# Kernel optimization log

Measured on AMD Instinct MI355X. Metric: run time of the kernel, lower is better.

## Reference

```python
import jax, jax.numpy as jnp
import numpy as np

DIM = 768
HEADS = 12
HEAD_DIM = DIM // HEADS
GRID = 32
MLP_HIDDEN = DIM * 4
EPS = 1e-5


def layernorm(x, g, b):
    m = jnp.mean(x, axis=-1, keepdims=True)
    v = jnp.mean((x - m) ** 2, axis=-1, keepdims=True)
    return (x - m) * jax.lax.rsqrt(v + EPS) * g + b


def geometry_bias(wg_w, wg_b):
    # Box-relational embedding on a GRIDxGRID grid; batch-invariant so computed once.
    g = GRID
    idx = jnp.arange(g, dtype=jnp.float32)
    px = jnp.repeat(idx, g) / g          # row index, normalized
    py = jnp.tile(idx, g) / g            # col index, normalized
    cx = px + 0.5 / g
    cy = py + 0.5 / g
    wbox = 1.0 + 1.0 / g                 # x_max - x_min + 1 (constant)
    dx = jnp.log(jnp.clip(jnp.abs((cx[:, None] - cx[None, :]) / wbox), 1e-3, None))
    dy = jnp.log(jnp.clip(jnp.abs((cy[:, None] - cy[None, :]) / wbox), 1e-3, None))
    dz = jnp.zeros_like(dx)              # log(w/w) = log(h/h) = 0
    pos = jnp.stack([dx, dy, dz, dz], axis=-1)                      # [N,N,4]
    dim_mat = 1.0 / (1000.0 ** (jnp.arange(8, dtype=jnp.float32) / 8.0))
    mul = (100.0 * pos)[..., None] * dim_mat                        # [N,N,4,8]
    mul = mul.reshape(g * g, g * g, 32)
    emb = jnp.concatenate([jnp.sin(mul), jnp.cos(mul)], axis=-1)    # [N,N,64]
    w = jax.nn.relu(jnp.einsum('ijd,hd->hij', emb, wg_w) + wg_b[:, None, None])
    rgw = jnp.log(jnp.clip(w, 1e-6, None))                          # [H,N,N]
    return jnp.pad(rgw, ((0, 0), (1, 0), (1, 0)))                   # zero row/col for cls


def mha(x, qkv_w, proj_w, proj_b, bias=None):
    Bt, N, C = x.shape
    qkv = (x @ qkv_w.T).reshape(Bt, N, 3, HEADS, HEAD_DIM).transpose(2, 0, 3, 1, 4)
    q, k, v = qkv[0], qkv[1], qkv[2]
    attn = jnp.einsum('bhid,bhjd->bhij', q, k) * (HEAD_DIM ** -0.5)
    if bias is not None:
        attn = attn + bias
    attn = jax.nn.softmax(attn, axis=-1)
    out = jnp.einsum('bhij,bhjd->bhid', attn, v).transpose(0, 2, 1, 3).reshape(Bt, N, C)
    return out @ proj_w.T + proj_b


def mlp(x, fc1_w, fc1_b, fc2_w, fc2_b):
    h = jax.nn.gelu(x @ fc1_w.T + fc1_b, approximate=False)
    return h @ fc2_w.T + fc2_b


def setup_inputs() -> dict:
    key = jax.random.key(0)
    ks = jax.random.split(key, 16)
    s = 0.02
    d = {
        'x': jax.random.normal(ks[0], (2, 4097, DIM), dtype=jnp.float32),
        'norm1_g': jnp.ones((DIM,), jnp.float32), 'norm1_b': jnp.zeros((DIM,), jnp.float32),
        'qkv_w': s * jax.random.normal(ks[1], (3 * DIM, DIM), dtype=jnp.float32),
        'proj_w': s * jax.random.normal(ks[2], (DIM, DIM), dtype=jnp.float32),
        'proj_b': jnp.zeros((DIM,), jnp.float32),
        'wg_w': s * jax.random.normal(ks[3], (HEADS, 64), dtype=jnp.float32),
        'wg_b': s * jax.random.normal(ks[4], (HEADS,), dtype=jnp.float32),
        'tnorm1_g': jnp.ones((DIM,), jnp.float32), 'tnorm1_b': jnp.zeros((DIM,), jnp.float32),
        'tqkv_w': s * jax.random.normal(ks[5], (3 * DIM, DIM), dtype=jnp.float32),
        'tproj_w': s * jax.random.normal(ks[6], (DIM, DIM), dtype=jnp.float32),
        'tproj_b': jnp.zeros((DIM,), jnp.float32),
        'tfc_w': s * jax.random.normal(ks[7], (DIM, DIM), dtype=jnp.float32),
        'tfc_b': jnp.zeros((DIM,), jnp.float32),
        'norm2_g': jnp.ones((DIM,), jnp.float32), 'norm2_b': jnp.zeros((DIM,), jnp.float32),
        'fc1_w': s * jax.random.normal(ks[8], (MLP_HIDDEN, DIM), dtype=jnp.float32),
        'fc1_b': jnp.zeros((MLP_HIDDEN,), jnp.float32),
        'fc2_w': s * jax.random.normal(ks[9], (DIM, MLP_HIDDEN), dtype=jnp.float32),
        'fc2_b': jnp.zeros((DIM,), jnp.float32),
        'B': 2, 'T': 4, 'W': 32,
    }
    return d


def reference(x, norm1_g, norm1_b, qkv_w, proj_w, proj_b, wg_w, wg_b,
              tnorm1_g, tnorm1_b, tqkv_w, tproj_w, tproj_b, tfc_w, tfc_b,
              norm2_g, norm2_b, fc1_w, fc1_b, fc2_w, fc2_b, B, T, W):
    m = x.shape[2]
    H = ((x.shape[1] - 1) // T) // W
    # temporal attention: b (h w t) m -> (b h w) t m
    xt = x[:, 1:, :]
    xt_t = xt.reshape(B, H, W, T, m).reshape(B * H * W, T, m)
    res_t = mha(layernorm(xt_t, tnorm1_g, tnorm1_b), tqkv_w, tproj_w, tproj_b)
    res_t = res_t.reshape(B, H, W, T, m).reshape(B, H * W * T, m)
    res_t = res_t @ tfc_w.T + tfc_b
    xt = x[:, 1:, :] + res_t
    # spatial attention with geometric bias: b (h w t) m -> (b t) (h w) m
    init_cls = x[:, 0:1, :]
    cls = jnp.broadcast_to(init_cls, (B, T, m)).reshape(B * T, 1, m)
    xs = xt.reshape(B, H, W, T, m).transpose(0, 3, 1, 2, 4).reshape(B * T, H * W, m)
    xs = jnp.concatenate([cls, xs], axis=1)
    bias = geometry_bias(wg_w, wg_b)[None]  # [1,heads,1+HW,1+HW]
    res_s = mha(layernorm(xs, norm1_g, norm1_b), qkv_w, proj_w, proj_b, bias=bias)
    cls_out = res_s[:, 0, :].reshape(B, T, m).mean(axis=1, keepdims=True)
    res_s = res_s[:, 1:, :].reshape(B, T, H, W, m).transpose(0, 2, 3, 1, 4).reshape(B, H * W * T, m)
    xout = jnp.concatenate([init_cls, xt], axis=1) + jnp.concatenate([cls_out, res_s], axis=1)
    xout = xout + mlp(layernorm(xout, norm2_g, norm2_b), fc1_w, fc1_b, fc2_w, fc2_b)
    return xout
```

## Files before the change

kernel.cpp:

```cpp
#include <hip/hip_runtime.h>
#include <stdint.h>

#define DIM   768
#define HEADS 12
#define NSP   1025
#define VT_LD 1152
#define PS_LD 136

typedef __attribute__((ext_vector_type(8))) short short8;
typedef __attribute__((ext_vector_type(4))) float f32x4;
typedef unsigned short u16;
typedef unsigned int   u32;

__device__ __forceinline__ u16 f2bf(float v) {
  u32 u = __builtin_bit_cast(u32, v);
  u += 0x7fffu + ((u >> 16) & 1u);
  return (u16)(u >> 16);
}
__device__ __forceinline__ float bf2f(u16 h) {
  u32 u = ((u32)h) << 16;
  return __builtin_bit_cast(float, u);
}

__device__ __forceinline__ void load_lds16(const u16* g, u16* lbase, int lane) {
#if __has_builtin(__builtin_amdgcn_global_load_lds)
  __builtin_amdgcn_global_load_lds((const __attribute__((address_space(1))) void*)g,
                                   (__attribute__((address_space(3))) void*)lbase, 16, 0, 0);
#else
  *(short8*)(lbase + lane * 8) = *(const short8*)g;
#endif
}

__global__ __launch_bounds__(256) void zero_k(float* __restrict__ o, long n) {
  long i = (long)blockIdx.x * 256 + threadIdx.x;
  if (i < n) o[i] = 0.0f;
}

__global__ __launch_bounds__(256) void cvt_k(const float* __restrict__ src,
                                             u16* __restrict__ dst, long n) {
  long i = (long)blockIdx.x * 256 + threadIdx.x;
  if (i < n) dst[i] = f2bf(src[i]);
}

__device__ __forceinline__ void ln_row(const float* __restrict__ src,
                                       u16* __restrict__ dst,
                                       const float* __restrict__ g,
                                       const float* __restrict__ b) {
  int tid = threadIdx.x;
  float v[3];
  float s = 0.f, ss = 0.f;
#pragma unroll
  for (int i = 0; i < 3; i++) {
    v[i] = src[tid + i * 256];
    s += v[i];
    ss += v[i] * v[i];
  }
  __shared__ float red[8];
#pragma unroll
  for (int m = 32; m; m >>= 1) {
    s  += __shfl_xor(s, m);
    ss += __shfl_xor(ss, m);
  }
  int wid = tid >> 6;
  if ((tid & 63) == 0) { red[wid] = s; red[4 + wid] = ss; }
  __syncthreads();
  s  = red[0] + red[1] + red[2] + red[3];
  ss = red[4] + red[5] + red[6] + red[7];
  float mean = s * (1.0f / 768.0f);
  float var  = ss * (1.0f / 768.0f) - mean * mean;
  float rs = rsqrtf(var + 1e-5f);
#pragma unroll
  for (int i = 0; i < 3; i++) {
    int c = tid + i * 256;
    dst[c] = f2bf((v[i] - mean) * rs * g[c] + b[c]);
  }
}

__global__ __launch_bounds__(256) void ln_xt_k(const float* __restrict__ x,
                                               const float* __restrict__ g,
                                               const float* __restrict__ b,
                                               u16* __restrict__ outb) {
  int q = blockIdx.x, bb = blockIdx.y;
  const float* src = x + ((long)bb * 4097 + 1 + q) * DIM;
  u16* dst = outb + ((long)bb * 4096 + q) * DIM;
  ln_row(src, dst, g, b);
}

__global__ __launch_bounds__(256) void ln_xs_k(const float* __restrict__ x,
                                               const float* __restrict__ xt,
                                               const float* __restrict__ g,
                                               const float* __restrict__ b,
                                               u16* __restrict__ outb) {
  int n = blockIdx.x, bt = blockIdx.y;
  int bb = bt >> 2, t = bt & 3;
  const float* src;
  if (n == 0) src = x + (long)bb * 4097 * DIM;
  else        src = xt + ((long)bb * 4096 + (long)(n - 1) * 4 + t) * DIM;
  u16* dst = outb + ((long)bt * NSP + n) * DIM;
  ln_row(src, dst, g, b);
}

__global__ __launch_bounds__(256) void ln2_k(const float* __restrict__ xo,
                                             const float* __restrict__ g,
                                             const float* __restrict__ b,
                                             u16* __restrict__ outb) {
  int n = blockIdx.x, bb = blockIdx.y;
  const float* src = xo + ((long)bb * 4097 + n) * DIM;
  u16* dst = outb + ((long)bb * 4097 + n) * DIM;
  ln_row(src, dst, g, b);
}

struct GemmParams {
  const u16* A; long lda, sA1;
  const u16* B; long ldb;
  void* C;      long ldc, sC1;
  const float* bias;
  const float* resid; long ldr, sR1;
  float scale;
  int M, N, K;
};

template <bool OUTBF16, bool BIASV, bool RESID, bool GELU_>
__global__ __launch_bounds__(256) void gemm_k(GemmParams p) {
  __shared__ u16 As[4096];
  __shared__ u16 Bs[4096];
  int tid = threadIdx.x;
  int z1 = blockIdx.z;
  const u16* A = p.A + (long)z1 * p.sA1;
  const u16* B = p.B;
  int m0 = blockIdx.y * 128, n0 = blockIdx.x * 128;
  int wave = tid >> 6, lane = tid & 63;
  int quad = lane >> 4, lrow = lane & 15;
  int wm = (wave & 1) * 64, wn = (wave >> 1) * 64;

  int rA0 = m0 + (tid >> 2);        if (rA0 > p.M - 1) rA0 = p.M - 1;
  int rA1 = m0 + 64 + (tid >> 2);   if (rA1 > p.M - 1) rA1 = p.M - 1;
  int rB0 = n0 + (tid >> 2);        if (rB0 > p.N - 1) rB0 = p.N - 1;
  int rB1 = n0 + 64 + (tid >> 2);   if (rB1 > p.N - 1) rB1 = p.N - 1;
  int c8 = (tid & 3) << 3;
  const u16* pa0 = A + (long)rA0 * p.lda + c8;
  const u16* pa1 = A + (long)rA1 * p.lda + c8;
  const u16* pb0 = B + (long)rB0 * p.ldb + c8;
  const u16* pb1 = B + (long)rB1 * p.ldb + c8;
  u16* lA0 = As + wave * 512;  u16* lA1 = As + 2048 + wave * 512;
  u16* lB0 = Bs + wave * 512;  u16* lB1 = Bs + 2048 + wave * 512;

  f32x4 acc[4][4];
#pragma unroll
  for (int i = 0; i < 4; i++)
#pragma unroll
    for (int j = 0; j < 4; j++) acc[i][j] = (f32x4){0.f, 0.f, 0.f, 0.f};

  for (int k0 = 0; k0 < p.K; k0 += 32) {
    load_lds16(pa0 + k0, lA0, lane);
    load_lds16(pa1 + k0, lA1, lane);
    load_lds16(pb0 + k0, lB0, lane);
    load_lds16(pb1 + k0, lB1, lane);
    __syncthreads();
    short8 af[4], bfr[4];
#pragma unroll
    for (int i = 0; i < 4; i++) af[i]  = *(const short8*)&As[(wm + i * 16 + lrow) * 32 + quad * 8];
#pragma unroll
    for (int j = 0; j < 4; j++) bfr[j] = *(const short8*)&Bs[(wn + j * 16 + lrow) * 32 + quad * 8];
#pragma unroll
    for (int i = 0; i < 4; i++)
#pragma unroll
      for (int j = 0; j < 4; j++)
        acc[i][j] = __builtin_amdgcn_mfma_f32_16x16x32_bf16(af[i], bfr[j], acc[i][j], 0, 0, 0);
    __syncthreads();
  }

  float* Cf = (float*)p.C;
  u16*   Ch = (u16*)p.C;
  long cbase = (long)z1 * p.sC1;
#pragma unroll
  for (int i = 0; i < 4; i++) {
    int rbase = m0 + wm + i * 16 + quad * 4;
#pragma unroll
    for (int j = 0; j < 4; j++) {
      int c = n0 + wn + j * 16 + lrow;
      if (c >= p.N) continue;
#pragma unroll
      for (int rr = 0; rr < 4; rr++) {
        int r = rbase + rr;
        if (r >= p.M) continue;
        float v = acc[i][j][rr] * p.scale;
        if (BIASV) v += p.bias[c];
        if (GELU_) v = 0.5f * v * (1.0f + erff(v * 0.70710678118654752f));
        if (RESID) v += p.resid[(long)z1 * p.sR1 + (long)r * p.ldr + c];
        long o = cbase + (long)r * p.ldc + c;
        if (OUTBF16) Ch[o] = f2bf(v);
        else         Cf[o] = v;
      }
    }
  }
}

__global__ __launch_bounds__(64) void attn_t_k(const u16* __restrict__ qkv,
                                               u16* __restrict__ outb) {
  int h = blockIdx.x;
  int g = blockIdx.y;
  int d = threadIdx.x;
  long base = (long)g * 4 * 2304 + h * 64 + d;
  float q[4], k[4], vv[4];
#pragma unroll
  for (int t = 0; t < 4; t++) {
    q[t]  = bf2f(qkv[base + (long)t * 2304]);
    k[t]  = bf2f(qkv[base + (long)t * 2304 + 768]);
    vv[t] = bf2f(qkv[base + (long)t * 2304 + 1536]);
  }
  float sc[4][4];
#pragma unroll
  for (int i = 0; i < 4; i++)
#pragma unroll
    for (int j = 0; j < 4; j++) {
      float pv = q[i] * k[j];
#pragma unroll
      for (int m = 32; m; m >>= 1) pv += __shfl_xor(pv, m);
      sc[i][j] = pv * 0.125f;
    }
#pragma unroll
  for (int i = 0; i < 4; i++) {
    float mx = fmaxf(fmaxf(sc[i][0], sc[i][1]), fmaxf(sc[i][2], sc[i][3]));
    float e0 = __expf(sc[i][0] - mx), e1 = __expf(sc[i][1] - mx);
    float e2 = __expf(sc[i][2] - mx), e3 = __expf(sc[i][3] - mx);
    float inv = 1.0f / (e0 + e1 + e2 + e3);
    float ov = (e0 * vv[0] + e1 * vv[1] + e2 * vv[2] + e3 * vv[3]) * inv;
    outb[((long)g * 4 + i) * DIM + h * 64 + d] = f2bf(ov);
  }
}

__global__ void geo_pre_k(const float* __restrict__ wg_w,
                          const float* __restrict__ wg_b,
                          float* __restrict__ sxsyc) {
  int t = threadIdx.x;
  if (t >= 384) return;
  int h = t >> 5, dd = t & 31;
  float dx = logf(fmaxf((float)dd * (1.0f / 33.0f), 0.001f));
  float sx = 0.f, sy = 0.f;
#pragma unroll
  for (int k2 = 0; k2 < 8; k2++) {
    float dm = powf(1000.0f, -(float)k2 / 8.0f);
    float a = 100.0f * dx * dm;
    float sn = sinf(a), cs = cosf(a);
    sx += sn * wg_w[h * 64 + k2]     + cs * wg_w[h * 64 + 32 + k2];
    sy += sn * wg_w[h * 64 + 8 + k2] + cs * wg_w[h * 64 + 40 + k2];
  }
  sxsyc[t] = sx;
  sxsyc[384 + t] = sy;
  if (dd == 0) {
    float c = wg_b[h];
#pragma unroll
    for (int k2 = 48; k2 < 64; k2++) c += wg_w[h * 64 + k2];
    sxsyc[768 + h] = c;
  }
}

__global__ __launch_bounds__(256) void geo_bias_k(const float* __restrict__ sxsyc,
                                                  float* __restrict__ Bh_g) {
  int h = blockIdx.x / 4;
  int idx = (blockIdx.x % 4) * 256 + threadIdx.x;
  int dr = idx >> 5, dc = idx & 31;
  float v = sxsyc[h * 32 + dr] + sxsyc[384 + h * 32 + dc] + sxsyc[768 + h];
  Bh_g[h * 1024 + idx] = logf(fmaxf(fmaxf(v, 0.0f), 1e-6f));
}

__global__ __launch_bounds__(256) void vtrans_k(const u16* __restrict__ qkv_s,
                                                u16* __restrict__ Vt) {
  __shared__ u16 tile[64][33];
  int bh = blockIdx.y;
  int bt = bh / 12, h = bh % 12;
  int j0 = blockIdx.x * 32;
  int tid = threadIdx.x;
#pragma unroll
  for (int it = 0; it < 8; it++) {
    int jj = it * 4 + (tid >> 6);
    int d = tid & 63;
    int j = j0 + jj;
    u16 v = 0;
    if (j < NSP) v = qkv_s[((long)bt * NSP + j) * 2304 + 1536 + h * 64 + d];
    tile[d][jj] = v;
  }
  __syncthreads();
#pragma unroll
  for (int it = 0; it < 8; it++) {
    int d = it * 8 + (tid >> 5);
    int j = tid & 31;
    Vt[((long)bh * 64 + d) * VT_LD + j0 + j] = tile[d][j];
  }
}

__global__ __launch_bounds__(256, 4) void attn_s_k(const u16* __restrict__ qkv,
                                                   const u16* __restrict__ Vt,
                                                   const float* __restrict__ Bh_g,
                                                   u16* __restrict__ attn_o) {
  __shared__ u16 KsF[8192];
  __shared__ u16 UN[8704];
  __shared__ float BhS[1024];
  const int qt = blockIdx.x, bh = blockIdx.y;
  const int bt = bh / 12, h = bh % 12;
  const int tid = threadIdx.x;
  const int wave = tid >> 6, lane = tid & 63;
  const int quad = lane >> 4, lr = lane & 15;
  const int m0 = qt * 64;
  const long qb = (long)bt * NSP * 2304 + h * 64;

#pragma unroll
  for (int i = 0; i < 4; i++) BhS[tid + i * 256] = Bh_g[h * 1024 + tid + i * 256];

  {
    int rowq = tid >> 2, colq = (tid & 3) << 3;
    int tokq = m0 + rowq; if (tokq > 1024) tokq = 1024;
    const u16* gq = qkv + qb + (long)tokq * 2304 + colq;
    load_lds16(gq,      UN + wave * 512, lane);
    load_lds16(gq + 32, UN + 2048 + wave * 512, lane);
  }
  __syncthreads();
  short8 qf[2];
#pragma unroll
  for (int ks = 0; ks < 2; ks++)
    qf[ks] = *(const short8*)&UN[ks * 2048 + (wave * 16 + lr) * 32 + quad * 8];

  f32x4 Oa[4];
  float mr[4], lsum[4];
#pragma unroll
  for (int n = 0; n < 4; n++) Oa[n] = (f32x4){0.f, 0.f, 0.f, 0.f};
#pragma unroll
  for (int r = 0; r < 4; r++) { mr[r] = -1e30f; lsum[r] = 0.f; }

  int rid[4], ri_[4], ci_[4];
  float rok[4];
#pragma unroll
  for (int r = 0; r < 4; r++) {
    int i0 = m0 + wave * 16 + quad * 4 + r;
    rid[r] = i0;
    int ii = i0 < NSP ? i0 : (NSP - 1);
    int im1 = ii > 0 ? ii - 1 : 0;
    ri_[r] = im1 >> 5;
    ci_[r] = im1 & 31;
    rok[r] = (i0 > 0) ? 1.0f : 0.0f;
  }

  int rowk = tid >> 2, colk = (tid & 3) << 3;

  for (int kt = 0; kt < 9; kt++) {
    __syncthreads();
    {
      int t0 = kt * 128 + rowk;      if (t0 > 1024) t0 = 1024;
      int t1 = kt * 128 + 64 + rowk; if (t1 > 1024) t1 = 1024;
      const u16* g0 = qkv + qb + 768 + (long)t0 * 2304 + colk;
      const u16* g1 = qkv + qb + 768 + (long)t1 * 2304 + colk;
      load_lds16(g0,      KsF + wave * 512, lane);
      load_lds16(g1,      KsF + 2048 + wave * 512, lane);
      load_lds16(g0 + 32, KsF + 4096 + wave * 512, lane);
      load_lds16(g1 + 32, KsF + 6144 + wave * 512, lane);
    }
    __syncthreads();
    f32x4 sa[8];
#pragma unroll
    for (int j = 0; j < 8; j++) sa[j] = (f32x4){0.f, 0.f, 0.f, 0.f};
#pragma unroll
    for (int ks = 0; ks < 2; ks++) {
#pragma unroll
      for (int j = 0; j < 8; j++) {
        short8 kf = *(const short8*)&KsF[ks * 4096 + (j * 16 + lr) * 32 + quad * 8];
        sa[j] = __builtin_amdgcn_mfma_f32_16x16x32_bf16(qf[ks], kf, sa[j], 0, 0, 0);
      }
    }
#pragma unroll
    for (int j = 0; j < 8; j++) {
      int j0 = kt * 128 + j * 16 + lr;
      bool jv = j0 < NSP;
      int jm1 = j0 > 0 ? j0 - 1 : 0;
      if (jm1 > 1023) jm1 = 1023;
      int rj = jm1 >> 5, cj = jm1 & 31;
      float jnz = (j0 > 0) ? 1.0f : 0.0f;
#pragma unroll
      for (int r = 0; r < 4; r++) {
        int ad = ri_[r] - rj; ad = ad < 0 ? -ad : ad;
        int cd = ci_[r] - cj; cd = cd < 0 ? -cd : cd;
        float sv = sa[j][r] * 0.125f + BhS[ad * 32 + cd] * jnz * rok[r];
        sa[j][r] = jv ? sv : -1e30f;
      }
    }
    float alpha[4];
#pragma unroll
    for (int r = 0; r < 4; r++) {
      float tm = sa[0][r];
#pragma unroll
      for (int j = 1; j < 8; j++) tm = fmaxf(tm, sa[j][r]);
      tm = fmaxf(tm, __shfl_xor(tm, 1));
      tm = fmaxf(tm, __shfl_xor(tm, 2));
      tm = fmaxf(tm, __shfl_xor(tm, 4));
      tm = fmaxf(tm, __shfl_xor(tm, 8));
      float mn = fmaxf(mr[r], tm);
      float a = __expf(mr[r] - mn);
      alpha[r] = a;
      float ls = 0.f;
      int prow = (wave * 16 + quad * 4 + r) * PS_LD;
#pragma unroll
      for (int j = 0; j < 8; j++) {
        float pp = __expf(sa[j][r] - mn);
        ls += pp;
        UN[prow + j * 16 + lr] = f2bf(pp);
      }
      lsum[r] = lsum[r] * a + ls;
      mr[r] = mn;
    }
#pragma unroll
    for (int n = 0; n < 4; n++)
#pragma unroll
      for (int r = 0; r < 4; r++) Oa[n][r] *= alpha[r];
#pragma unroll
    for (int ks = 0; ks < 4; ks++) {
      short8 pf = *(const short8*)&UN[(wave * 16 + lr) * PS_LD + ks * 32 + quad * 8];
#pragma unroll
      for (int n = 0; n < 4; n++) {
        short8 vf = *(const short8*)(Vt + ((long)bh * 64 + n * 16 + lr) * VT_LD + kt * 128 + ks * 32 + quad * 8);
        Oa[n] = __builtin_amdgcn_mfma_f32_16x16x32_bf16(pf, vf, Oa[n], 0, 0, 0);
      }
    }
  }
#pragma unroll
  for (int r = 0; r < 4; r++) {
    float l = lsum[r];
    l += __shfl_xor(l, 1);
    l += __shfl_xor(l, 2);
    l += __shfl_xor(l, 4);
    l += __shfl_xor(l, 8);
    lsum[r] = 1.0f / l;
  }
#pragma unroll
  for (int r = 0; r < 4; r++) {
    int i0 = rid[r];
    if (i0 < NSP) {
      long ob = ((long)bt * NSP + i0) * 768 + h * 64;
#pragma unroll
      for (int n = 0; n < 4; n++)
        attn_o[ob + n * 16 + lr] = f2bf(Oa[n][r] * lsum[r]);
    }
  }
}

__global__ __launch_bounds__(256) void assemble_k(const float* __restrict__ x,
                                                  const float* __restrict__ xt,
                                                  const float* __restrict__ res_s,
                                                  float* __restrict__ outp) {
  int n = blockIdx.x, bb = blockIdx.y;
  int tid = threadIdx.x;
  long ob = ((long)bb * 4097 + n) * DIM;
  if (n == 0) {
#pragma unroll
    for (int i = 0; i < 3; i++) {
      int c = tid + i * 256;
      float acc = x[ob + c];
#pragma unroll
      for (int t = 0; t < 4; t++)
        acc += 0.25f * res_s[((long)(bb * 4 + t) * NSP) * DIM + c];
      outp[ob + c] = acc;
    }
  } else {
    int q = n - 1, hw = q >> 2, t = q & 3;
    long rs = ((long)(bb * 4 + t) * NSP + 1 + hw) * DIM;
    long xb = ((long)bb * 4096 + q) * DIM;
#pragma unroll
    for (int i = 0; i < 3; i++) {
      int c = tid + i * 256;
      outp[ob + c] = xt[xb + c] + res_s[rs + c];
    }
  }
}

extern "C" void kernel_launch(void* const* d_in, const int* in_sizes, int n_in,
                              void* d_out, int out_size, void* d_ws, size_t ws_size,
                              hipStream_t stream) {
  const float* x        = (const float*)d_in[0];
  const float* norm1_g  = (const float*)d_in[1];
  const float* norm1_b  = (const float*)d_in[2];
  const float* qkv_w    = (const float*)d_in[3];
  const float* proj_w   = (const float*)d_in[4];
  const float* proj_b   = (const float*)d_in[5];
  const float* wg_w     = (const float*)d_in[6];
  const float* wg_b     = (const float*)d_in[7];
  const float* tnorm1_g = (const float*)d_in[8];
  const float* tnorm1_b = (const float*)d_in[9];
  const float* tqkv_w   = (const float*)d_in[10];
  const float* tproj_w  = (const float*)d_in[11];
  const float* tproj_b  = (const float*)d_in[12];
  const float* tfc_w    = (const float*)d_in[13];
  const float* tfc_b    = (const float*)d_in[14];
  const float* norm2_g  = (const float*)d_in[15];
  const float* norm2_b  = (const float*)d_in[16];
  const float* fc1_w    = (const float*)d_in[17];
  const float* fc1_b    = (const float*)d_in[18];
  const float* fc2_w    = (const float*)d_in[19];
  const float* fc2_b    = (const float*)d_in[20];
  float* out = (float*)d_out;
  (void)in_sizes; (void)n_in; (void)out_size;

  char* base = (char*)d_ws;
  size_t off = 0;
  auto take = [&](size_t bytes) -> char* {
    char* p = base + off;
    off += (bytes + 255) & ~(size_t)255;
    return p;
  };

  u16* wb_tqkv = (u16*)take(2304LL * 768 * 2);
  u16* wb_tprj = (u16*)take(768LL * 768 * 2);
  u16* wb_tfc  = (u16*)take(768LL * 768 * 2);
  u16* wb_qkv  = (u16*)take(2304LL * 768 * 2);
  u16* wb_proj = (u16*)take(768LL * 768 * 2);
  u16* wb_fc1  = (u16*)take(3072LL * 768 * 2);
  u16* wb_fc2  = (u16*)take(3072LL * 768 * 2);
  float* xt_f  = (float*)take(8192LL * 768 * 4);
  float* sxsyc = (float*)take(4096);
  float* Bh_g  = (float*)take(12LL * 1024 * 4);
  char* pool   = take(64536576);
  size_t REQ = off;

  u16* qkv_t  = (u16*)(pool);
  u16* ln_xt  = (u16*)(pool + 37748736);
  u16* attn_t = ln_xt;
  u16* h1     = (u16*)(pool + 50331648);
  u16* qkv_s  = (u16*)(pool);
  u16* ln_xs  = (u16*)(pool + 37785600);
  u16* attn_sp = ln_xs;
  u16* Vt     = (u16*)(pool + 50380800);
  float* res_s = (float*)(pool);
  u16* ln2b   = (u16*)(pool);
  u16* geluh  = (u16*)(pool + 12585984);

  if (ws_size < REQ) {
    long n = 2LL * 4097 * 768;
    zero_k<<<dim3((n + 255) / 256), 256, 0, stream>>>(out, n);
    return;
  }

  {
    struct { const float* s; u16* d; long n; } cv[7] = {
      {tqkv_w, wb_tqkv, 2304LL * 768}, {tproj_w, wb_tprj, 768LL * 768},
      {tfc_w, wb_tfc, 768LL * 768},    {qkv_w, wb_qkv, 2304LL * 768},
      {proj_w, wb_proj, 768LL * 768},  {fc1_w, wb_fc1, 3072LL * 768},
      {fc2_w, wb_fc2, 3072LL * 768}};
    for (int i = 0; i < 7; i++)
      cvt_k<<<dim3((cv[i].n + 255) / 256), 256, 0, stream>>>(cv[i].s, cv[i].d, cv[i].n);
  }
  geo_pre_k<<<1, 384, 0, stream>>>(wg_w, wg_b, sxsyc);
  geo_bias_k<<<48, 256, 0, stream>>>(sxsyc, Bh_g);

  ln_xt_k<<<dim3(4096, 2), 256, 0, stream>>>(x, tnorm1_g, tnorm1_b, ln_xt);
  {
    GemmParams p{};
    p.A = ln_xt; p.lda = 768; p.B = wb_tqkv; p.ldb = 768;
    p.C = qkv_t; p.ldc = 2304; p.scale = 1.0f;
    p.M = 8192; p.N = 2304; p.K = 768;
    gemm_k<true, false, false, false><<<dim3(18, 64, 1), 256, 0, stream>>>(p);
  }
  attn_t_k<<<dim3(12, 2048), 64, 0, stream>>>(qkv_t, attn_t);
  {
    GemmParams p{};
    p.A = attn_t; p.lda = 768; p.B = wb_tprj; p.ldb = 768;
    p.C = h1; p.ldc = 768; p.bias = tproj_b; p.scale = 1.0f;
    p.M = 8192; p.N = 768; p.K = 768;
    gemm_k<true, true, false, false><<<dim3(6, 64, 1), 256, 0, stream>>>(p);
  }
  {
    GemmParams p{};
    p.A = h1; p.lda = 768; p.sA1 = 4096LL * 768;
    p.B = wb_tfc; p.ldb = 768;
    p.C = xt_f; p.ldc = 768; p.sC1 = 4096LL * 768;
    p.bias = tfc_b;
    p.resid = x + 768; p.ldr = 768; p.sR1 = 4097LL * 768;
    p.scale = 1.0f;
    p.M = 4096; p.N = 768; p.K = 768;
    gemm_k<false, true, true, false><<<dim3(6, 32, 2), 256, 0, stream>>>(p);
  }

  ln_xs_k<<<dim3(NSP, 8), 256, 0, stream>>>(x, xt_f, norm1_g, norm1_b, ln_xs);
  {
    GemmParams p{};
    p.A = ln_xs; p.lda = 768; p.B = wb_qkv; p.ldb = 768;
    p.C = qkv_s; p.ldc = 2304; p.scale = 1.0f;
    p.M = 8200; p.N = 2304; p.K = 768;
    gemm_k<true, false, false, false><<<dim3(18, 65, 1), 256, 0, stream>>>(p);
  }
  vtrans_k<<<dim3(36, 96), 256, 0, stream>>>(qkv_s, Vt);
  attn_s_k<<<dim3(17, 96), 256, 0, stream>>>(qkv_s, Vt, Bh_g, attn_sp);
  {
    GemmParams p{};
    p.A = attn_sp; p.lda = 768; p.B = wb_proj; p.ldb = 768;
    p.C = res_s; p.ldc = 768; p.bias = proj_b; p.scale = 1.0f;
    p.M = 8200; p.N = 768; p.K = 768;
    gemm_k<false, true, false, false><<<dim3(6, 65, 1), 256, 0, stream>>>(p);
  }
  assemble_k<<<dim3(4097, 2), 256, 0, stream>>>(x, xt_f, res_s, out);

  ln2_k<<<dim3(4097, 2), 256, 0, stream>>>(out, norm2_g, norm2_b, ln2b);
  {
    GemmParams p{};
    p.A = ln2b; p.lda = 768; p.B = wb_fc1; p.ldb = 768;
    p.C = geluh; p.ldc = 3072; p.bias = fc1_b; p.scale = 1.0f;
    p.M = 8194; p.N = 3072; p.K = 768;
    gemm_k<true, true, false, true><<<dim3(24, 65, 1), 256, 0, stream>>>(p);
  }
  {
    GemmParams p{};
    p.A = geluh; p.lda = 3072; p.B = wb_fc2; p.ldb = 3072;
    p.C = out; p.ldc = 768; p.bias = fc2_b;
    p.resid = out; p.ldr = 768; p.scale = 1.0f;
    p.M = 8194; p.N = 768; p.K = 3072;
    gemm_k<false, true, true, false><<<dim3(6, 65, 1), 256, 0, stream>>>(p);
  }
}
```

Before: 818.0 us.

## Add 64-wide GEMM tiles, double-buffer spatial attention K, fuse assemble with LayerNorm

Adds an NT64 GEMM variant with 128x64 output tiles, used for the N=768 projections so they launch more blocks and fill more CUs. The spatial attention kernel now processes 64-key tiles with double-buffered K loads in LDS, prefetches V fragments into registers, and uses a flat grid that interleaves heads across blocks. The residual assemble step is fused with the second LayerNorm, which removes one full read of the output. Risks include a lower MFMA-to-load ratio in the narrow GEMM tiles and an extra barrier on each attention tile iteration.

```diff
diff --git a/kernel.cpp b/kernel.cpp
--- a/kernel.cpp
+++ b/kernel.cpp
@@ -5,7 +5,7 @@
 #define HEADS 12
 #define NSP   1025
 #define VT_LD 1152
-#define PS_LD 136
+#define PS_LD 72
 
 typedef __attribute__((ext_vector_type(8))) short short8;
 typedef __attribute__((ext_vector_type(4))) float f32x4;
@@ -100,16 +100,6 @@
   ln_row(src, dst, g, b);
 }
 
-__global__ __launch_bounds__(256) void ln2_k(const float* __restrict__ xo,
-                                             const float* __restrict__ g,
-                                             const float* __restrict__ b,
-                                             u16* __restrict__ outb) {
-  int n = blockIdx.x, bb = blockIdx.y;
-  const float* src = xo + ((long)bb * 4097 + n) * DIM;
-  u16* dst = outb + ((long)bb * 4097 + n) * DIM;
-  ln_row(src, dst, g, b);
-}
-
 struct GemmParams {
   const u16* A; long lda, sA1;
   const u16* B; long ldb;
@@ -120,52 +110,64 @@
   int M, N, K;
 };
 
-template <bool OUTBF16, bool BIASV, bool RESID, bool GELU_>
+template <bool OUTBF16, bool BIASV, bool RESID, bool GELU_, bool NT64>
 __global__ __launch_bounds__(256) void gemm_k(GemmParams p) {
+  constexpr int NJ = NT64 ? 2 : 4;
   __shared__ u16 As[4096];
-  __shared__ u16 Bs[4096];
+  __shared__ u16 Bs[NT64 ? 2048 : 4096];
   int tid = threadIdx.x;
   int z1 = blockIdx.z;
   const u16* A = p.A + (long)z1 * p.sA1;
   const u16* B = p.B;
-  int m0 = blockIdx.y * 128, n0 = blockIdx.x * 128;
+  int m0 = blockIdx.y * 128, n0 = blockIdx.x * (NT64 ? 64 : 128);
   int wave = tid >> 6, lane = tid & 63;
   int quad = lane >> 4, lrow = lane & 15;
-  int wm = (wave & 1) * 64, wn = (wave >> 1) * 64;
+  int wm = (wave & 1) * 64;
+  int wn = NT64 ? (wave >> 1) * 32 : (wave >> 1) * 64;
 
   int rA0 = m0 + (tid >> 2);        if (rA0 > p.M - 1) rA0 = p.M - 1;
   int rA1 = m0 + 64 + (tid >> 2);   if (rA1 > p.M - 1) rA1 = p.M - 1;
-  int rB0 = n0 + (tid >> 2);        if (rB0 > p.N - 1) rB0 = p.N - 1;
-  int rB1 = n0 + 64 + (tid >> 2);   if (rB1 > p.N - 1) rB1 = p.N - 1;
   int c8 = (tid & 3) << 3;
   const u16* pa0 = A + (long)rA0 * p.lda + c8;
   const u16* pa1 = A + (long)rA1 * p.lda + c8;
-  const u16* pb0 = B + (long)rB0 * p.ldb + c8;
-  const u16* pb1 = B + (long)rB1 * p.ldb + c8;
   u16* lA0 = As + wave * 512;  u16* lA1 = As + 2048 + wave * 512;
-  u16* lB0 = Bs + wave * 512;  u16* lB1 = Bs + 2048 + wave * 512;
-
-  f32x4 acc[4][4];
+
+  const u16 *pb0, *pb1 = nullptr;
+  u16 *lB0, *lB1 = nullptr;
+  {
+    int rB0 = n0 + (tid >> 2);
+    if (!NT64) {
+      int rB1 = n0 + 64 + (tid >> 2);
+      if (rB0 > p.N - 1) rB0 = p.N - 1;
+      if (rB1 > p.N - 1) rB1 = p.N - 1;
+      pb1 = B + (long)rB1 * p.ldb + c8;
+      lB1 = Bs + 2048 + wave * 512;
+    }
+    pb0 = B + (long)rB0 * p.ldb + c8;
+    lB0 = Bs + wave * 512;
+  }
+
+  f32x4 acc[4][NJ];
 #pragma unroll
   for (int i = 0; i < 4; i++)
 #pragma unroll
-    for (int j = 0; j < 4; j++) acc[i][j] = (f32x4){0.f, 0.f, 0.f, 0.f};
+    for (int j = 0; j < NJ; j++) acc[i][j] = (f32x4){0.f, 0.f, 0.f, 0.f};
 
   for (int k0 = 0; k0 < p.K; k0 += 32) {
     load_lds16(pa0 + k0, lA0, lane);
     load_lds16(pa1 + k0, lA1, lane);
     load_lds16(pb0 + k0, lB0, lane);
-    load_lds16(pb1 + k0, lB1, lane);
+    if (!NT64) load_lds16(pb1 + k0, lB1, lane);
     __syncthreads();
-    short8 af[4], bfr[4];
-#pragma unroll
-    for (int i = 0; i < 4; i++) af[i]  = *(const short8*)&As[(wm + i * 16 + lrow) * 32 + quad * 8];
-#pragma unroll
-    for (int j = 0; j < 4; j++) bfr[j] = *(const short8*)&Bs[(wn + j * 16 + lrow) * 32 + quad * 8];
+    short8 af[4], bfr[NJ];
+#pragma unroll
+    for (int i = 0; i < 4; i++)  af[i]  = *(const short8*)&As[(wm + i * 16 + lrow) * 32 + quad * 8];
+#pragma unroll
+    for (int j = 0; j < NJ; j++) bfr[j] = *(const short8*)&Bs[(wn + j * 16 + lrow) * 32 + quad * 8];
 #pragma unroll
     for (int i = 0; i < 4; i++)
 #pragma unroll
-      for (int j = 0; j < 4; j++)
+      for (int j = 0; j < NJ; j++)
         acc[i][j] = __builtin_amdgcn_mfma_f32_16x16x32_bf16(af[i], bfr[j], acc[i][j], 0, 0, 0);
     __syncthreads();
   }
@@ -177,7 +179,7 @@
   for (int i = 0; i < 4; i++) {
     int rbase = m0 + wm + i * 16 + quad * 4;
 #pragma unroll
-    for (int j = 0; j < 4; j++) {
+    for (int j = 0; j < NJ; j++) {
       int c = n0 + wn + j * 16 + lrow;
       if (c >= p.N) continue;
 #pragma unroll
@@ -295,9 +297,12 @@
                                                    const float* __restrict__ Bh_g,
                                                    u16* __restrict__ attn_o) {
   __shared__ u16 KsF[8192];
-  __shared__ u16 UN[8704];
+  __shared__ u16 UN[4608];
   __shared__ float BhS[1024];
-  const int qt = blockIdx.x, bh = blockIdx.y;
+  const int bid = blockIdx.x;
+  const int slot = bid >> 3;
+  const int bh = (bid & 7) * 12 + slot / 17;
+  const int qt = slot % 17;
   const int bt = bh / 12, h = bh % 12;
   const int tid = threadIdx.x;
   const int wave = tid >> 6, lane = tid & 63;
@@ -308,12 +313,18 @@
 #pragma unroll
   for (int i = 0; i < 4; i++) BhS[tid + i * 256] = Bh_g[h * 1024 + tid + i * 256];
 
-  {
-    int rowq = tid >> 2, colq = (tid & 3) << 3;
+  const int rowq = tid >> 2, colq = (tid & 3) << 3;
+  {
     int tokq = m0 + rowq; if (tokq > 1024) tokq = 1024;
     const u16* gq = qkv + qb + (long)tokq * 2304 + colq;
     load_lds16(gq,      UN + wave * 512, lane);
     load_lds16(gq + 32, UN + 2048 + wave * 512, lane);
+  }
+  {
+    int t0 = rowq; if (t0 > 1024) t0 = 1024;
+    const u16* g0 = qkv + qb + 768 + (long)t0 * 2304 + colq;
+    load_lds16(g0,      KsF + wave * 512, lane);
+    load_lds16(g0 + 32, KsF + 2048 + wave * 512, lane);
   }
   __syncthreads();
   short8 qf[2];
@@ -341,35 +352,37 @@
     rok[r] = (i0 > 0) ? 1.0f : 0.0f;
   }
 
-  int rowk = tid >> 2, colk = (tid & 3) << 3;
-
-  for (int kt = 0; kt < 9; kt++) {
-    __syncthreads();
-    {
-      int t0 = kt * 128 + rowk;      if (t0 > 1024) t0 = 1024;
-      int t1 = kt * 128 + 64 + rowk; if (t1 > 1024) t1 = 1024;
-      const u16* g0 = qkv + qb + 768 + (long)t0 * 2304 + colk;
-      const u16* g1 = qkv + qb + 768 + (long)t1 * 2304 + colk;
-      load_lds16(g0,      KsF + wave * 512, lane);
-      load_lds16(g1,      KsF + 2048 + wave * 512, lane);
-      load_lds16(g0 + 32, KsF + 4096 + wave * 512, lane);
-      load_lds16(g1 + 32, KsF + 6144 + wave * 512, lane);
-    }
-    __syncthreads();
-    f32x4 sa[8];
-#pragma unroll
-    for (int j = 0; j < 8; j++) sa[j] = (f32x4){0.f, 0.f, 0.f, 0.f};
+  const u16* vrow = Vt + ((long)bh * 64 + lr) * VT_LD;
+
+  for (int kt = 0; kt < 17; kt++) {
+    const int cur = kt & 1, nxt = cur ^ 1;
+    if (kt < 16) {
+      int t0 = (kt + 1) * 64 + rowq; if (t0 > 1024) t0 = 1024;
+      const u16* g0 = qkv + qb + 768 + (long)t0 * 2304 + colq;
+      load_lds16(g0,      KsF + nxt * 4096 + wave * 512, lane);
+      load_lds16(g0 + 32, KsF + nxt * 4096 + 2048 + wave * 512, lane);
+    }
+    short8 vf0[4], vf1[4];
+#pragma unroll
+    for (int n = 0; n < 4; n++)
+      vf0[n] = *(const short8*)(vrow + (long)n * 16 * VT_LD + kt * 64 + quad * 8);
+    f32x4 sa[4];
+#pragma unroll
+    for (int j = 0; j < 4; j++) sa[j] = (f32x4){0.f, 0.f, 0.f, 0.f};
 #pragma unroll
     for (int ks = 0; ks < 2; ks++) {
 #pragma unroll
-      for (int j = 0; j < 8; j++) {
-        short8 kf = *(const short8*)&KsF[ks * 4096 + (j * 16 + lr) * 32 + quad * 8];
+      for (int j = 0; j < 4; j++) {
+        short8 kf = *(const short8*)&KsF[cur * 4096 + ks * 2048 + (j * 16 + lr) * 32 + quad * 8];
         sa[j] = __builtin_amdgcn_mfma_f32_16x16x32_bf16(qf[ks], kf, sa[j], 0, 0, 0);
       }
     }
 #pragma unroll
-    for (int j = 0; j < 8; j++) {
-      int j0 = kt * 128 + j * 16 + lr;
+    for (int n = 0; n < 4; n++)
+      vf1[n] = *(const short8*)(vrow + (long)n * 16 * VT_LD + kt * 64 + 32 + quad * 8);
+#pragma unroll
+    for (int j = 0; j < 4; j++) {
+      int j0 = kt * 64 + j * 16 + lr;
       bool jv = j0 < NSP;
       int jm1 = j0 > 0 ? j0 - 1 : 0;
       if (jm1 > 1023) jm1 = 1023;
@@ -386,9 +399,7 @@
     float alpha[4];
 #pragma unroll
     for (int r = 0; r < 4; r++) {
-      float tm = sa[0][r];
-#pragma unroll
-      for (int j = 1; j < 8; j++) tm = fmaxf(tm, sa[j][r]);
+      float tm = fmaxf(fmaxf(sa[0][r], sa[1][r]), fmaxf(sa[2][r], sa[3][r]));
       tm = fmaxf(tm, __shfl_xor(tm, 1));
       tm = fmaxf(tm, __shfl_xor(tm, 2));
       tm = fmaxf(tm, __shfl_xor(tm, 4));
@@ -399,7 +410,7 @@
       float ls = 0.f;
       int prow = (wave * 16 + quad * 4 + r) * PS_LD;
 #pragma unroll
-      for (int j = 0; j < 8; j++) {
+      for (int j = 0; j < 4; j++) {
         float pp = __expf(sa[j][r] - mn);
         ls += pp;
         UN[prow + j * 16 + lr] = f2bf(pp);
@@ -412,14 +423,13 @@
 #pragma unroll
       for (int r = 0; r < 4; r++) Oa[n][r] *= alpha[r];
 #pragma unroll
-    for (int ks = 0; ks < 4; ks++) {
+    for (int ks = 0; ks < 2; ks++) {
       short8 pf = *(const short8*)&UN[(wave * 16 + lr) * PS_LD + ks * 32 + quad * 8];
 #pragma unroll
-      for (int n = 0; n < 4; n++) {
-        short8 vf = *(const short8*)(Vt + ((long)bh * 64 + n * 16 + lr) * VT_LD + kt * 128 + ks * 32 + quad * 8);
-        Oa[n] = __builtin_amdgcn_mfma_f32_16x16x32_bf16(pf, vf, Oa[n], 0, 0, 0);
-      }
-    }
+      for (int n = 0; n < 4; n++)
+        Oa[n] = __builtin_amdgcn_mfma_f32_16x16x32_bf16(pf, ks ? vf1[n] : vf0[n], Oa[n], 0, 0, 0);
+    }
+    __syncthreads();
   }
 #pragma unroll
   for (int r = 0; r < 4; r++) {
@@ -442,13 +452,17 @@
   }
 }
 
-__global__ __launch_bounds__(256) void assemble_k(const float* __restrict__ x,
-                                                  const float* __restrict__ xt,
-                                                  const float* __restrict__ res_s,
-                                                  float* __restrict__ outp) {
+__global__ __launch_bounds__(256) void assemble_ln_k(const float* __restrict__ x,
+                                                     const float* __restrict__ xt,
+                                                     const float* __restrict__ res_s,
+                                                     const float* __restrict__ g,
+                                                     const float* __restrict__ b,
+                                                     float* __restrict__ outp,
+                                                     u16* __restrict__ ln2b) {
   int n = blockIdx.x, bb = blockIdx.y;
   int tid = threadIdx.x;
   long ob = ((long)bb * 4097 + n) * DIM;
+  float val[3];
   if (n == 0) {
 #pragma unroll
     for (int i = 0; i < 3; i++) {
@@ -457,7 +471,7 @@
 #pragma unroll
       for (int t = 0; t < 4; t++)
         acc += 0.25f * res_s[((long)(bb * 4 + t) * NSP) * DIM + c];
-      outp[ob + c] = acc;
+      val[i] = acc;
     }
   } else {
     int q = n - 1, hw = q >> 2, t = q & 3;
@@ -466,8 +480,34 @@
 #pragma unroll
     for (int i = 0; i < 3; i++) {
       int c = tid + i * 256;
-      outp[ob + c] = xt[xb + c] + res_s[rs + c];
-    }
+      val[i] = xt[xb + c] + res_s[rs + c];
+    }
+  }
+  float s = 0.f, ss = 0.f;
+#pragma unroll
+  for (int i = 0; i < 3; i++) {
+    outp[ob + tid + i * 256] = val[i];
+    s += val[i];
+    ss += val[i] * val[i];
+  }
+  __shared__ float red[8];
+#pragma unroll
+  for (int m = 32; m; m >>= 1) {
+    s  += __shfl_xor(s, m);
+    ss += __shfl_xor(ss, m);
+  }
+  int wid = tid >> 6;
+  if ((tid & 63) == 0) { red[wid] = s; red[4 + wid] = ss; }
+  __syncthreads();
+  s  = red[0] + red[1] + red[2] + red[3];
+  ss = red[4] + red[5] + red[6] + red[7];
+  float mean = s * (1.0f / 768.0f);
+  float var  = ss * (1.0f / 768.0f) - mean * mean;
+  float rs = rsqrtf(var + 1e-5f);
+#pragma unroll
+  for (int i = 0; i < 3; i++) {
+    int c = tid + i * 256;
+    ln2b[ob + c] = f2bf((val[i] - mean) * rs * g[c] + b[c]);
   }
 }
 
@@ -527,8 +567,8 @@
   u16* ln_xs  = (u16*)(pool + 37785600);
   u16* attn_sp = ln_xs;
   u16* Vt     = (u16*)(pool + 50380800);
-  float* res_s = (float*)(pool);
   u16* ln2b   = (u16*)(pool);
+  float* res_s = (float*)(pool + 12585984);
   u16* geluh  = (u16*)(pool + 12585984);
 
   if (ws_size < REQ) {
@@ -555,7 +595,7 @@
     p.A = ln_xt; p.lda = 768; p.B = wb_tqkv; p.ldb = 768;
     p.C = qkv_t; p.ldc = 2304; p.scale = 1.0f;
     p.M = 8192; p.N = 2304; p.K = 768;
-    gemm_k<true, false, false, false><<<dim3(18, 64, 1), 256, 0, stream>>>(p);
+    gemm_k<true, false, false, false, false><<<dim3(18, 64, 1), 256, 0, stream>>>(p);
   }
   attn_t_k<<<dim3(12, 2048), 64, 0, stream>>>(qkv_t, attn_t);
   {
@@ -563,7 +603,7 @@
     p.A = attn_t; p.lda = 768; p.B = wb_tprj; p.ldb = 768;
     p.C = h1; p.ldc = 768; p.bias = tproj_b; p.scale = 1.0f;
     p.M = 8192; p.N = 768; p.K = 768;
-    gemm_k<true, true, false, false><<<dim3(6, 64, 1), 256, 0, stream>>>(p);
+    gemm_k<true, true, false, false, true><<<dim3(12, 64, 1), 256, 0, stream>>>(p);
   }
   {
     GemmParams p{};
@@ -574,7 +614,7 @@
     p.resid = x + 768; p.ldr = 768; p.sR1 = 4097LL * 768;
     p.scale = 1.0f;
     p.M = 4096; p.N = 768; p.K = 768;
-    gemm_k<false, true, true, false><<<dim3(6, 32, 2), 256, 0, stream>>>(p);
+    gemm_k<false, true, true, false, true><<<dim3(12, 32, 2), 256, 0, stream>>>(p);
   }
 
   ln_xs_k<<<dim3(NSP, 8), 256, 0, stream>>>(x, xt_f, norm1_g, norm1_b, ln_xs);
@@ -583,26 +623,25 @@
     p.A = ln_xs; p.lda = 768; p.B = wb_qkv; p.ldb = 768;
     p.C = qkv_s; p.ldc = 2304; p.scale = 1.0f;
     p.M = 8200; p.N = 2304; p.K = 768;
-    gemm_k<true, false, false, false><<<dim3(18, 65, 1), 256, 0, stream>>>(p);
+    gemm_k<true, false, false, false, false><<<dim3(18, 65, 1), 256, 0, stream>>>(p);
   }
   vtrans_k<<<dim3(36, 96), 256, 0, stream>>>(qkv_s, Vt);
-  attn_s_k<<<dim3(17, 96), 256, 0, stream>>>(qkv_s, Vt, Bh_g, attn_sp);
+  attn_s_k<<<dim3(1632), 256, 0, stream>>>(qkv_s, Vt, Bh_g, attn_sp);
   {
     GemmParams p{};
     p.A = attn_sp; p.lda = 768; p.B = wb_proj; p.ldb = 768;
     p.C = res_s; p.ldc = 768; p.bias = proj_b; p.scale = 1.0f;
     p.M = 8200; p.N = 768; p.K = 768;
-    gemm_k<false, true, false, false><<<dim3(6, 65, 1), 256, 0, stream>>>(p);
-  }
-  assemble_k<<<dim3(4097, 2), 256, 0, stream>>>(x, xt_f, res_s, out);
-
-  ln2_k<<<dim3(4097, 2), 256, 0, stream>>>(out, norm2_g, norm2_b, ln2b);
+    gemm_k<false, true, false, false, true><<<dim3(12, 65, 1), 256, 0, stream>>>(p);
+  }
+  assemble_ln_k<<<dim3(4097, 2), 256, 0, stream>>>(x, xt_f, res_s, norm2_g, norm2_b, out, ln2b);
+
   {
     GemmParams p{};
     p.A = ln2b; p.lda = 768; p.B = wb_fc1; p.ldb = 768;
     p.C = geluh; p.ldc = 3072; p.bias = fc1_b; p.scale = 1.0f;
     p.M = 8194; p.N = 3072; p.K = 768;
-    gemm_k<true, true, false, true><<<dim3(24, 65, 1), 256, 0, stream>>>(p);
+    gemm_k<true, true, false, true, false><<<dim3(24, 65, 1), 256, 0, stream>>>(p);
   }
   {
     GemmParams p{};
@@ -610,6 +649,6 @@
     p.C = out; p.ldc = 768; p.bias = fc2_b;
     p.resid = out; p.ldr = 768; p.scale = 1.0f;
     p.M = 8194; p.N = 768; p.K = 3072;
-    gemm_k<false, true, true, false><<<dim3(6, 65, 1), 256, 0, stream>>>(p);
-  }
-}
+    gemm_k<false, true, true, false, true><<<dim3(12, 65, 1), 256, 0, stream>>>(p);
+  }
+}
```

Result: faster. 744.9 us (-8.9%).
